# Performance work log

Hardware: AMD Instinct MI355X
Metric: run time of the kernel (lower is better)

Reference implementation:

```python
import jax, jax.numpy as jnp
import numpy as np

B, S, H, OUT, L = 32, 4096, 128, 128, 3


def _log_g(x):
    return jnp.where(x >= 0, jnp.log(jax.nn.relu(x) + 0.5), -jax.nn.softplus(-x))


def _cell(x, Wz, bz, Wh, bh):
    # x: [B, S, Din] -> h: [B, S, H]
    k = x @ Wz.T + bz                              # [B,S,H]
    log_z = -jax.nn.softplus(-k)
    log_coeffs = -jax.nn.softplus(k)
    # h_0 = zeros -> log_g(0) = log(0.5)
    log_h0 = jnp.full((x.shape[0], 1, k.shape[-1]), np.log(0.5), dtype=k.dtype)
    log_tilde_h = _log_g(x @ Wh.T + bh)
    log_values = jnp.concatenate([log_h0, log_z + log_tilde_h], axis=1)  # [B,S+1,H]
    # FAITHFUL to source: cumsum over the FEATURE axis (dim=-1), pad along seq
    a_star = jnp.pad(jnp.cumsum(log_coeffs, axis=-1), ((0, 0), (1, 0), (0, 0)))
    log_h = a_star + jax.lax.cumlogsumexp(log_values - a_star, axis=1)
    # torch forward applies sigmoid to the cell output, then drops the h_0 row
    return jax.nn.sigmoid(jnp.exp(log_h))[:, 1:, :]


def setup_inputs() -> dict:
    key = jax.random.key(0)
    ks = jax.random.split(key, 2 * L + 2)
    inp = {"x": jax.random.normal(ks[0], (B, S), dtype=jnp.float32)}
    for l in range(L):
        din = 1 if l == 0 else H
        inp[f"Wz{l}"] = jax.random.normal(ks[1 + 2 * l], (H, din), dtype=jnp.float32) * 0.02
        inp[f"bz{l}"] = jnp.zeros((H,), dtype=jnp.float32)
        inp[f"Wh{l}"] = jax.random.normal(ks[2 + 2 * l], (H, din), dtype=jnp.float32) * 0.02
        inp[f"bh{l}"] = jnp.zeros((H,), dtype=jnp.float32)
    inp["Wout"] = jax.random.normal(ks[-1], (OUT, H * S), dtype=jnp.float32) * (1.0 / np.sqrt(H * S))
    inp["bout"] = jnp.zeros((OUT,), dtype=jnp.float32)
    return inp


def reference(x, Wz0, bz0, Wh0, bh0, Wz1, bz1, Wh1, bh1, Wz2, bz2, Wh2, bh2, Wout, bout):
    h = x[:, :, None]  # [B,S,1]
    for (Wz, bz, Wh, bh) in ((Wz0, bz0, Wh0, bh0), (Wz1, bz1, Wh1, bh1), (Wz2, bz2, Wh2, bh2)):
        h = _cell(h, Wz, bz, Wh, bh)
    flat = h.reshape(h.shape[0], -1)  # [B, S*H]
    return flat @ Wout.T + bout       # [B, OUT]
```

## Files before the change

kernel.cpp:

```cpp
#include <hip/hip_runtime.h>
#include <hip/hip_bf16.h>
#include <math.h>

#define B_   32
#define S_   4096
#define H_   128
#define OUT_ 128
#define P_   (B_*S_)
#define NC_  64
#define CH_  (S_/NC_)
#define NKS_ 1024
#define KTOT_ (H_*S_)
#define NEGINF_ (-__builtin_inff())
#define HTP_ 136
#define LOGHALF_ (-0.6931471805599453f)

typedef __bf16 bf16x8 __attribute__((ext_vector_type(8)));
typedef float  f32x4  __attribute__((ext_vector_type(4)));
typedef unsigned short ushort8_t __attribute__((ext_vector_type(8)));

__device__ __forceinline__ float sp_(float x) {
  return __logf(1.f + __expf(x));
}
__device__ __forceinline__ float logg_(float x) {
  float t = (x >= 0.f) ? (x + 0.5f) : __builtin_amdgcn_rcpf(1.f + __expf(-x));
  return __logf(t);
}
__device__ __forceinline__ float lae_(float a, float b) {
  float m = fmaxf(a, b);
  float d = -fabsf(a - b);
  return m + __logf(1.f + __expf(d));
}
__device__ __forceinline__ float sigm_(float e) {
  return __builtin_amdgcn_rcpf(1.f + __expf(-e));
}
__device__ __forceinline__ unsigned short f2bf_(float f) {
  unsigned int u = __float_as_uint(f);
  u += 0x7fffu + ((u >> 16) & 1u);
  return (unsigned short)(u >> 16);
}

#define DPPADD_(v, ctrl, rmask) \
  ((v) + __int_as_float(__builtin_amdgcn_update_dpp( \
      0, __float_as_int(v), (ctrl), (rmask), 0xf, true)))
__device__ __forceinline__ float wscan_(float v) {
  v = DPPADD_(v, 0x111, 0xf);
  v = DPPADD_(v, 0x112, 0xf);
  v = DPPADD_(v, 0x114, 0xf);
  v = DPPADD_(v, 0x118, 0xf);
  v = DPPADD_(v, 0x142, 0xa);
  v = DPPADD_(v, 0x143, 0xc);
  return v;
}

__global__ __launch_bounds__(256) void prep0c_kernel(
    const float* __restrict__ x,
    const float* __restrict__ Wz, const float* __restrict__ bz,
    const float* __restrict__ Wh, const float* __restrict__ bh,
    float* __restrict__ Lb, float* __restrict__ A, float* __restrict__ tot,
    const float* __restrict__ Wz1, const float* __restrict__ Wh1,
    const float* __restrict__ Wz2, const float* __restrict__ Wh2,
    unsigned short* __restrict__ Wc1, unsigned short* __restrict__ Wc2)
{
  __shared__ float segw[4][128];
  if (blockIdx.x >= 2048) {
    int idx = (blockIdx.x - 2048) * 256 + threadIdx.x;
    Wc1[idx] = f2bf_(idx < 16384 ? Wz1[idx] : Wh1[idx - 16384]);
    Wc2[idx] = f2bf_(idx < 16384 ? Wz2[idx] : Wh2[idx - 16384]);
    return;
  }
  int lane = threadIdx.x & 63, w = threadIdx.x >> 6;
  float wz0 = Wz[lane], wz1 = Wz[lane + 64];
  float bz0 = bz[lane], bz1 = bz[lane + 64];
  float wh0 = Wh[lane], wh1 = Wh[lane + 64];
  float bh0 = bh[lane], bh1 = bh[lane + 64];
  int blk = blockIdx.x;
  size_t base = (size_t)blk * (CH_ * H_);
  int pos0 = blk * CH_ + w * 16;
  float xv[16];
  #pragma unroll
  for (int j = 0; j < 16; ++j) xv[j] = x[pos0 + j];
  float L0[16], L1[16];
  float r0 = NEGINF_, r1 = NEGINF_;
  #pragma unroll
  for (int j = 0; j < 16; ++j) {
    float k0 = fmaf(xv[j], wz0, bz0), k1 = fmaf(xv[j], wz1, bz1);
    float g0 = fmaf(xv[j], wh0, bh0), g1 = fmaf(xv[j], wh1, bh1);
    float lc0 = -sp_(k0), lc1 = -sp_(k1);
    float lv0 = k0 + lc0 + logg_(g0);
    float lv1 = k1 + lc1 + logg_(g1);
    float s0 = wscan_(lc0);
    float c0 = __shfl(s0, 63, 64);
    float s1 = wscan_(lc1) + c0;
    float u0 = lv0 - s0, u1 = lv1 - s1;
    r0 = lae_(r0, u0); r1 = lae_(r1, u1);
    L0[j] = r0; L1[j] = r1;
    size_t o = base + (size_t)(w * 16 + j) * H_;
    A[o + lane] = s0; A[o + 64 + lane] = s1;
  }
  segw[w][lane] = r0; segw[w][lane + 64] = r1;
  __syncthreads();
  float p0 = NEGINF_, p1 = NEGINF_;
  for (int jj = 0; jj < w; ++jj) {
    p0 = lae_(p0, segw[jj][lane]);
    p1 = lae_(p1, segw[jj][lane + 64]);
  }
  #pragma unroll
  for (int j = 0; j < 16; ++j) {
    size_t o = base + (size_t)(w * 16 + j) * H_;
    Lb[o + lane]      = lae_(p0, L0[j]);
    Lb[o + 64 + lane] = lae_(p1, L1[j]);
  }
  if (w == 0) {
    float q0 = lae_(lae_(segw[0][lane], segw[1][lane]),
                    lae_(segw[2][lane], segw[3][lane]));
    float q1 = lae_(lae_(segw[0][lane + 64], segw[1][lane + 64]),
                    lae_(segw[2][lane + 64], segw[3][lane + 64]));
    tot[(size_t)blk * H_ + lane] = q0;
    tot[(size_t)blk * H_ + 64 + lane] = q1;
  }
}

__global__ __launch_bounds__(256) void kb_kernel(
    const float* __restrict__ totIn,
    const unsigned short* __restrict__ Wc,
    const float* __restrict__ bz, const float* __restrict__ bh,
    float* __restrict__ Lb, float* __restrict__ A,
    float* __restrict__ totOut)
{
  __shared__ unsigned short hT[64][HTP_];
  __shared__ float kg[16][260];
  __shared__ float segw[4][128];
  int tid = threadIdx.x;
  int lane = tid & 63, w = tid >> 6;
  int l15 = lane & 15, quad = lane >> 4;
  int half = tid >> 7, ch = tid & 127;
  int blk = blockIdx.x;
  int cidx = blk & (NC_ - 1);
  size_t base = (size_t)blk * (CH_ * H_);

  {
    const float* tp = totIn + (size_t)(blk - cidx) * H_ + ch;
    float p0 = NEGINF_, p1 = NEGINF_;
    int i = half;
    for (; i + 2 < cidx; i += 4) {
      float a0 = tp[(size_t)i * H_];
      float a1 = tp[(size_t)(i + 2) * H_];
      p0 = lae_(p0, a0); p1 = lae_(p1, a1);
    }
    for (; i < cidx; i += 2) p0 = lae_(p0, tp[(size_t)i * H_]);
    segw[half * 2][ch] = p0; segw[half * 2 + 1][ch] = p1;
  }
  __syncthreads();

  {
    float r = LOGHALF_;
    r = lae_(r, segw[0][ch]); r = lae_(r, segw[1][ch]);
    r = lae_(r, segw[2][ch]); r = lae_(r, segw[3][ch]);
    const float* Lp = Lb + base + (size_t)half * 32 * H_ + ch;
    const float* Ap = A  + base + (size_t)half * 32 * H_ + ch;
    for (int i0 = 0; i0 < 32; i0 += 16) {
      float Lv[16], Av[16];
      #pragma unroll
      for (int i = 0; i < 16; ++i) { Lv[i] = Lp[(i0 + i) * H_]; Av[i] = Ap[(i0 + i) * H_]; }
      #pragma unroll
      for (int i = 0; i < 16; ++i) {
        hT[half * 32 + i0 + i][ch] = f2bf_(sigm_(__expf(Av[i] + lae_(r, Lv[i]))));
      }
    }
  }
  __syncthreads();

  float bz0v = bz[lane], bz1v = bz[lane + 64];
  float bh0v = bh[lane], bh1v = bh[lane + 64];
  float R0 = NEGINF_, R1 = NEGINF_;

  for (int t = 0; t < 4; ++t) {
    f32x4 z = {0.f, 0.f, 0.f, 0.f};
    f32x4 acc[4] = {z, z, z, z};
    #pragma unroll
    for (int kk = 0; kk < 4; ++kk) {
      bf16x8 a = *reinterpret_cast<const bf16x8*>(&hT[t * 16 + l15][kk * 32 + quad * 8]);
      #pragma unroll
      for (int nt = 0; nt < 4; ++nt) {
        int n = w * 64 + nt * 16 + l15;
        bf16x8 bf = *reinterpret_cast<const bf16x8*>(Wc + n * 128 + kk * 32 + quad * 8);
        acc[nt] = __builtin_amdgcn_mfma_f32_16x16x32_bf16(a, bf, acc[nt], 0, 0, 0);
      }
    }
    __syncthreads();
    #pragma unroll
    for (int nt = 0; nt < 4; ++nt) {
      int col = w * 64 + nt * 16 + l15;
      #pragma unroll
      for (int r2 = 0; r2 < 4; ++r2)
        kg[quad * 4 + r2][col] = acc[nt][r2];
    }
    __syncthreads();
    float ll0[4], ll1[4];
    float lr0 = NEGINF_, lr1 = NEGINF_;
    #pragma unroll
    for (int i = 0; i < 4; ++i) {
      int row = w * 4 + i;
      int sIdx = t * 16 + row;
      float k0 = kg[row][lane]        + bz0v;
      float k1 = kg[row][64 + lane]   + bz1v;
      float g0 = kg[row][128 + lane]  + bh0v;
      float g1 = kg[row][192 + lane]  + bh1v;
      float lc0 = -sp_(k0), lc1 = -sp_(k1);
      float lv0 = k0 + lc0 + logg_(g0);
      float lv1 = k1 + lc1 + logg_(g1);
      float s0 = wscan_(lc0);
      float c0 = __shfl(s0, 63, 64);
      float s1 = wscan_(lc1) + c0;
      float u0 = lv0 - s0, u1 = lv1 - s1;
      lr0 = lae_(lr0, u0); lr1 = lae_(lr1, u1);
      ll0[i] = lr0; ll1[i] = lr1;
      size_t o = base + (size_t)sIdx * H_;
      A[o + lane] = s0;  A[o + 64 + lane] = s1;
    }
    segw[w][lane] = lr0; segw[w][lane + 64] = lr1;
    __syncthreads();
    float p0 = R0, p1 = R1;
    for (int jj = 0; jj < w; ++jj) {
      p0 = lae_(p0, segw[jj][lane]);
      p1 = lae_(p1, segw[jj][lane + 64]);
    }
    #pragma unroll
    for (int i = 0; i < 4; ++i) {
      size_t o = base + (size_t)(t * 16 + w * 4 + i) * H_;
      Lb[o + lane]      = lae_(p0, ll0[i]);
      Lb[o + 64 + lane] = lae_(p1, ll1[i]);
    }
    R0 = lae_(R0, lae_(lae_(segw[0][lane], segw[1][lane]),
                       lae_(segw[2][lane], segw[3][lane])));
    R1 = lae_(R1, lae_(lae_(segw[0][lane + 64], segw[1][lane + 64]),
                       lae_(segw[2][lane + 64], segw[3][lane + 64])));
  }

  if (w == 0) {
    totOut[(size_t)blk * H_ + lane] = R0;
    totOut[(size_t)blk * H_ + 64 + lane] = R1;
  }
}

__global__ __launch_bounds__(256) void scan3v2_kernel(
    const float* __restrict__ Lb, const float* __restrict__ A,
    const float* __restrict__ totIn, unsigned short* __restrict__ hbf)
{
  __shared__ float tpart[4][128];
  int tid = threadIdx.x;
  int half = tid >> 7, ch = tid & 127;
  int blk = blockIdx.x;
  int cidx = blk & (NC_ - 1);
  size_t base = (size_t)blk * (CH_ * H_);

  {
    const float* tp = totIn + (size_t)(blk - cidx) * H_ + ch;
    float p0 = NEGINF_, p1 = NEGINF_;
    int i = half;
    for (; i + 2 < cidx; i += 4) {
      float a0 = tp[(size_t)i * H_];
      float a1 = tp[(size_t)(i + 2) * H_];
      p0 = lae_(p0, a0); p1 = lae_(p1, a1);
    }
    for (; i < cidx; i += 2) p0 = lae_(p0, tp[(size_t)i * H_]);
    tpart[half * 2][ch] = p0; tpart[half * 2 + 1][ch] = p1;
  }
  __syncthreads();

  float r = LOGHALF_;
  r = lae_(r, tpart[0][ch]); r = lae_(r, tpart[1][ch]);
  r = lae_(r, tpart[2][ch]); r = lae_(r, tpart[3][ch]);
  const float* Lp = Lb + base + (size_t)half * 32 * H_ + ch;
  const float* Ap = A  + base + (size_t)half * 32 * H_ + ch;
  unsigned short* hp = hbf + base + (size_t)half * 32 * H_ + ch;
  for (int i0 = 0; i0 < 32; i0 += 16) {
    float Lv[16], Av[16];
    #pragma unroll
    for (int i = 0; i < 16; ++i) { Lv[i] = Lp[(i0 + i) * H_]; Av[i] = Ap[(i0 + i) * H_]; }
    #pragma unroll
    for (int i = 0; i < 16; ++i) {
      hp[(size_t)(i0 + i) * H_] = f2bf_(sigm_(__expf(Av[i] + lae_(r, Lv[i]))));
    }
  }
}

__global__ __launch_bounds__(256) void outmm_kernel(
    const unsigned short* __restrict__ hbf,
    const float* __restrict__ Wout,
    float* __restrict__ part)
{
  const int KSL = KTOT_ / NKS_;
  int tid = threadIdx.x, w = tid >> 6, lane = tid & 63;
  int l15 = lane & 15, quad = lane >> 4;
  int k0base = blockIdx.x * KSL;
  f32x4 acc[2][2] = {{{0,0,0,0},{0,0,0,0}},{{0,0,0,0},{0,0,0,0}}};
  for (int ks = 0; ks < KSL; ks += 32) {
    int k0 = k0base + ks;
    bf16x8 a0 = *reinterpret_cast<const bf16x8*>(
        hbf + (size_t)l15 * KTOT_ + k0 + quad * 8);
    bf16x8 a1 = *reinterpret_cast<const bf16x8*>(
        hbf + (size_t)(16 + l15) * KTOT_ + k0 + quad * 8);
    #pragma unroll
    for (int nt = 0; nt < 2; ++nt) {
      int n = w * 32 + nt * 16 + l15;
      const float* wp = Wout + (size_t)n * KTOT_ + k0 + quad * 8;
      float4 wa = *reinterpret_cast<const float4*>(wp);
      float4 wb = *reinterpret_cast<const float4*>(wp + 4);
      ushort8_t tt;
      tt[0] = f2bf_(wa.x); tt[1] = f2bf_(wa.y); tt[2] = f2bf_(wa.z); tt[3] = f2bf_(wa.w);
      tt[4] = f2bf_(wb.x); tt[5] = f2bf_(wb.y); tt[6] = f2bf_(wb.z); tt[7] = f2bf_(wb.w);
      bf16x8 bf = __builtin_bit_cast(bf16x8, tt);
      acc[0][nt] = __builtin_amdgcn_mfma_f32_16x16x32_bf16(a0, bf, acc[0][nt], 0, 0, 0);
      acc[1][nt] = __builtin_amdgcn_mfma_f32_16x16x32_bf16(a1, bf, acc[1][nt], 0, 0, 0);
    }
  }
  float* pp = part + (size_t)blockIdx.x * (B_ * OUT_);
  #pragma unroll
  for (int mt = 0; mt < 2; ++mt)
    #pragma unroll
    for (int nt = 0; nt < 2; ++nt)
      #pragma unroll
      for (int r = 0; r < 4; ++r) {
        int b = mt * 16 + quad * 4 + r;
        int o = w * 32 + nt * 16 + l15;
        pp[b * OUT_ + o] = acc[mt][nt][r];
      }
}

__global__ __launch_bounds__(256) void outred_kernel(
    const float* __restrict__ part, const float* __restrict__ bout,
    float* __restrict__ out)
{
  int w = threadIdx.x >> 6, lane = threadIdx.x & 63;
  int idx = blockIdx.x * 4 + w;
  float s = 0.f;
  for (int wg = lane; wg < NKS_; wg += 64) s += part[(size_t)wg * (B_ * OUT_) + idx];
  #pragma unroll
  for (int d = 32; d; d >>= 1) s += __shfl_down(s, (unsigned)d, 64);
  if (lane == 0) out[idx] = s + bout[idx & (OUT_ - 1)];
}

extern "C" void kernel_launch(void* const* d_in, const int* in_sizes, int n_in,
                              void* d_out, int out_size, void* d_ws, size_t ws_size,
                              hipStream_t stream)
{
  const float* x    = (const float*)d_in[0];
  const float* Wz[3] = {(const float*)d_in[1], (const float*)d_in[5], (const float*)d_in[9]};
  const float* bz[3] = {(const float*)d_in[2], (const float*)d_in[6], (const float*)d_in[10]};
  const float* Wh[3] = {(const float*)d_in[3], (const float*)d_in[7], (const float*)d_in[11]};
  const float* bh[3] = {(const float*)d_in[4], (const float*)d_in[8], (const float*)d_in[12]};
  const float* Wout = (const float*)d_in[13];
  const float* bout = (const float*)d_in[14];
  float* out = (float*)d_out;

  char* ws = (char*)d_ws;
  float*          Lb    = (float*)(ws + 0);
  float*          A     = (float*)(ws + 67108864);
  unsigned short* hbf   = (unsigned short*)(ws + 134217728);
  unsigned short* Wc1   = (unsigned short*)(ws + 167772160);
  unsigned short* Wc2   = (unsigned short*)(ws + 167837696);
  float*          totA  = (float*)(ws + 167903232);
  float*          totB  = (float*)(ws + 168951808);
  float*          part  = (float*)(ws + 0);

  prep0c_kernel<<<B_ * NC_ + 128, 256, 0, stream>>>(
      x, Wz[0], bz[0], Wh[0], bh[0], Lb, A, totA,
      Wz[1], Wh[1], Wz[2], Wh[2], Wc1, Wc2);

  kb_kernel<<<B_ * NC_, 256, 0, stream>>>(totA, Wc1, bz[1], bh[1], Lb, A, totB);
  kb_kernel<<<B_ * NC_, 256, 0, stream>>>(totB, Wc2, bz[2], bh[2], Lb, A, totA);

  scan3v2_kernel<<<B_ * NC_, 256, 0, stream>>>(Lb, A, totA, hbf);

  outmm_kernel<<<NKS_, 256, 0, stream>>>(hbf, Wout, part);
  outred_kernel<<<(B_ * OUT_) / 4, 256, 0, stream>>>(part, bout, out);
}
```

Measured before the change: 681.5 us.

## Recompute layer-0 scan in layer-1 kernel and fuse final scan into output GEMM

The first kernel now only computes per-chunk totals for layer 0 instead of writing the full Lb/A arrays. The layer-1 kernel recomputes the layer-0 cell from x in registers and applies the carry directly. The final-layer scan application moves into the output matmul, which reads Lb/A plus a precomputed per-chunk carry and builds bf16 activations on the fly, removing the hbf round trip. The cost is recomputing layer 0 and reading fp32 Lb/A (twice the bytes of bf16) inside the matmul, plus one extra small carry kernel.

```diff
diff --git a/kernel.cpp b/kernel.cpp
--- a/kernel.cpp
+++ b/kernel.cpp
@@ -53,11 +53,11 @@
   return v;
 }
 
-__global__ __launch_bounds__(256) void prep0c_kernel(
+__global__ __launch_bounds__(256) void tot0c_kernel(
     const float* __restrict__ x,
     const float* __restrict__ Wz, const float* __restrict__ bz,
     const float* __restrict__ Wh, const float* __restrict__ bh,
-    float* __restrict__ Lb, float* __restrict__ A, float* __restrict__ tot,
+    float* __restrict__ tot,
     const float* __restrict__ Wz1, const float* __restrict__ Wh1,
     const float* __restrict__ Wz2, const float* __restrict__ Wh2,
     unsigned short* __restrict__ Wc1, unsigned short* __restrict__ Wc2)
@@ -75,42 +75,23 @@
   float wh0 = Wh[lane], wh1 = Wh[lane + 64];
   float bh0 = bh[lane], bh1 = bh[lane + 64];
   int blk = blockIdx.x;
-  size_t base = (size_t)blk * (CH_ * H_);
   int pos0 = blk * CH_ + w * 16;
-  float xv[16];
-  #pragma unroll
-  for (int j = 0; j < 16; ++j) xv[j] = x[pos0 + j];
-  float L0[16], L1[16];
   float r0 = NEGINF_, r1 = NEGINF_;
   #pragma unroll
   for (int j = 0; j < 16; ++j) {
-    float k0 = fmaf(xv[j], wz0, bz0), k1 = fmaf(xv[j], wz1, bz1);
-    float g0 = fmaf(xv[j], wh0, bh0), g1 = fmaf(xv[j], wh1, bh1);
+    float xv = x[pos0 + j];
+    float k0 = fmaf(xv, wz0, bz0), k1 = fmaf(xv, wz1, bz1);
+    float g0 = fmaf(xv, wh0, bh0), g1 = fmaf(xv, wh1, bh1);
     float lc0 = -sp_(k0), lc1 = -sp_(k1);
     float lv0 = k0 + lc0 + logg_(g0);
     float lv1 = k1 + lc1 + logg_(g1);
     float s0 = wscan_(lc0);
     float c0 = __shfl(s0, 63, 64);
     float s1 = wscan_(lc1) + c0;
-    float u0 = lv0 - s0, u1 = lv1 - s1;
-    r0 = lae_(r0, u0); r1 = lae_(r1, u1);
-    L0[j] = r0; L1[j] = r1;
-    size_t o = base + (size_t)(w * 16 + j) * H_;
-    A[o + lane] = s0; A[o + 64 + lane] = s1;
+    r0 = lae_(r0, lv0 - s0); r1 = lae_(r1, lv1 - s1);
   }
   segw[w][lane] = r0; segw[w][lane + 64] = r1;
   __syncthreads();
-  float p0 = NEGINF_, p1 = NEGINF_;
-  for (int jj = 0; jj < w; ++jj) {
-    p0 = lae_(p0, segw[jj][lane]);
-    p1 = lae_(p1, segw[jj][lane + 64]);
-  }
-  #pragma unroll
-  for (int j = 0; j < 16; ++j) {
-    size_t o = base + (size_t)(w * 16 + j) * H_;
-    Lb[o + lane]      = lae_(p0, L0[j]);
-    Lb[o + 64 + lane] = lae_(p1, L1[j]);
-  }
   if (w == 0) {
     float q0 = lae_(lae_(segw[0][lane], segw[1][lane]),
                     lae_(segw[2][lane], segw[3][lane]));
@@ -121,8 +102,11 @@
   }
 }
 
-__global__ __launch_bounds__(256) void kb_kernel(
-    const float* __restrict__ totIn,
+__global__ __launch_bounds__(256) void kb1_kernel(
+    const float* __restrict__ x,
+    const float* __restrict__ Wz0, const float* __restrict__ bz0,
+    const float* __restrict__ Wh0, const float* __restrict__ bh0,
+    const float* __restrict__ tot0,
     const unsigned short* __restrict__ Wc,
     const float* __restrict__ bz, const float* __restrict__ bh,
     float* __restrict__ Lb, float* __restrict__ A,
@@ -131,42 +115,68 @@
   __shared__ unsigned short hT[64][HTP_];
   __shared__ float kg[16][260];
   __shared__ float segw[4][128];
+  __shared__ float pre[4][128];
   int tid = threadIdx.x;
   int lane = tid & 63, w = tid >> 6;
   int l15 = lane & 15, quad = lane >> 4;
-  int half = tid >> 7, ch = tid & 127;
+  int halfsel = tid >> 7, chh = tid & 127;
   int blk = blockIdx.x;
   int cidx = blk & (NC_ - 1);
   size_t base = (size_t)blk * (CH_ * H_);
 
   {
-    const float* tp = totIn + (size_t)(blk - cidx) * H_ + ch;
+    const float* tp = tot0 + (size_t)(blk - cidx) * H_ + chh;
     float p0 = NEGINF_, p1 = NEGINF_;
-    int i = half;
+    int i = halfsel;
     for (; i + 2 < cidx; i += 4) {
       float a0 = tp[(size_t)i * H_];
       float a1 = tp[(size_t)(i + 2) * H_];
       p0 = lae_(p0, a0); p1 = lae_(p1, a1);
     }
     for (; i < cidx; i += 2) p0 = lae_(p0, tp[(size_t)i * H_]);
-    segw[half * 2][ch] = p0; segw[half * 2 + 1][ch] = p1;
+    pre[halfsel * 2][chh] = p0; pre[halfsel * 2 + 1][chh] = p1;
   }
   __syncthreads();
 
   {
-    float r = LOGHALF_;
-    r = lae_(r, segw[0][ch]); r = lae_(r, segw[1][ch]);
-    r = lae_(r, segw[2][ch]); r = lae_(r, segw[3][ch]);
-    const float* Lp = Lb + base + (size_t)half * 32 * H_ + ch;
-    const float* Ap = A  + base + (size_t)half * 32 * H_ + ch;
-    for (int i0 = 0; i0 < 32; i0 += 16) {
-      float Lv[16], Av[16];
-      #pragma unroll
-      for (int i = 0; i < 16; ++i) { Lv[i] = Lp[(i0 + i) * H_]; Av[i] = Ap[(i0 + i) * H_]; }
-      #pragma unroll
-      for (int i = 0; i < 16; ++i) {
-        hT[half * 32 + i0 + i][ch] = f2bf_(sigm_(__expf(Av[i] + lae_(r, Lv[i]))));
-      }
+    float rA = LOGHALF_, rB = LOGHALF_;
+    rA = lae_(rA, pre[0][lane]); rA = lae_(rA, pre[1][lane]);
+    rA = lae_(rA, pre[2][lane]); rA = lae_(rA, pre[3][lane]);
+    rB = lae_(rB, pre[0][lane + 64]); rB = lae_(rB, pre[1][lane + 64]);
+    rB = lae_(rB, pre[2][lane + 64]); rB = lae_(rB, pre[3][lane + 64]);
+    float wz0 = Wz0[lane], wz1 = Wz0[lane + 64];
+    float bzz0 = bz0[lane], bzz1 = bz0[lane + 64];
+    float wh0 = Wh0[lane], wh1 = Wh0[lane + 64];
+    float bhh0 = bh0[lane], bhh1 = bh0[lane + 64];
+    int pos0 = blk * CH_ + w * 16;
+    float L0[16], L1[16], av0[16], av1[16];
+    float r0 = NEGINF_, r1 = NEGINF_;
+    #pragma unroll
+    for (int j = 0; j < 16; ++j) {
+      float xv = x[pos0 + j];
+      float k0 = fmaf(xv, wz0, bzz0), k1 = fmaf(xv, wz1, bzz1);
+      float g0 = fmaf(xv, wh0, bhh0), g1 = fmaf(xv, wh1, bhh1);
+      float lc0 = -sp_(k0), lc1 = -sp_(k1);
+      float lv0 = k0 + lc0 + logg_(g0);
+      float lv1 = k1 + lc1 + logg_(g1);
+      float s0 = wscan_(lc0);
+      float c0 = __shfl(s0, 63, 64);
+      float s1 = wscan_(lc1) + c0;
+      float u0 = lv0 - s0, u1 = lv1 - s1;
+      r0 = lae_(r0, u0); r1 = lae_(r1, u1);
+      L0[j] = r0; L1[j] = r1; av0[j] = s0; av1[j] = s1;
+    }
+    segw[w][lane] = r0; segw[w][lane + 64] = r1;
+    __syncthreads();
+    float p0 = rA, p1 = rB;
+    for (int jj = 0; jj < w; ++jj) {
+      p0 = lae_(p0, segw[jj][lane]);
+      p1 = lae_(p1, segw[jj][lane + 64]);
+    }
+    #pragma unroll
+    for (int j = 0; j < 16; ++j) {
+      hT[w * 16 + j][lane]      = f2bf_(sigm_(__expf(av0[j] + lae_(p0, L0[j]))));
+      hT[w * 16 + j][lane + 64] = f2bf_(sigm_(__expf(av1[j] + lae_(p1, L1[j]))));
     }
   }
   __syncthreads();
@@ -202,7 +212,6 @@
     #pragma unroll
     for (int i = 0; i < 4; ++i) {
       int row = w * 4 + i;
-      int sIdx = t * 16 + row;
       float k0 = kg[row][lane]        + bz0v;
       float k1 = kg[row][64 + lane]   + bz1v;
       float g0 = kg[row][128 + lane]  + bh0v;
@@ -216,7 +225,7 @@
       float u0 = lv0 - s0, u1 = lv1 - s1;
       lr0 = lae_(lr0, u0); lr1 = lae_(lr1, u1);
       ll0[i] = lr0; ll1[i] = lr1;
-      size_t o = base + (size_t)sIdx * H_;
+      size_t o = base + (size_t)(t * 16 + row) * H_;
       A[o + lane] = s0;  A[o + 64 + lane] = s1;
     }
     segw[w][lane] = lr0; segw[w][lane + 64] = lr1;
@@ -244,12 +253,19 @@
   }
 }
 
-__global__ __launch_bounds__(256) void scan3v2_kernel(
-    const float* __restrict__ Lb, const float* __restrict__ A,
-    const float* __restrict__ totIn, unsigned short* __restrict__ hbf)
-{
-  __shared__ float tpart[4][128];
+__global__ __launch_bounds__(256) void kb2_kernel(
+    const float* __restrict__ totIn,
+    const unsigned short* __restrict__ Wc,
+    const float* __restrict__ bz, const float* __restrict__ bh,
+    float* __restrict__ Lb, float* __restrict__ A,
+    float* __restrict__ totOut)
+{
+  __shared__ unsigned short hT[64][HTP_];
+  __shared__ float kg[16][260];
+  __shared__ float segw[4][128];
   int tid = threadIdx.x;
+  int lane = tid & 63, w = tid >> 6;
+  int l15 = lane & 15, quad = lane >> 4;
   int half = tid >> 7, ch = tid & 127;
   int blk = blockIdx.x;
   int cidx = blk & (NC_ - 1);
@@ -265,43 +281,170 @@
       p0 = lae_(p0, a0); p1 = lae_(p1, a1);
     }
     for (; i < cidx; i += 2) p0 = lae_(p0, tp[(size_t)i * H_]);
-    tpart[half * 2][ch] = p0; tpart[half * 2 + 1][ch] = p1;
+    segw[half * 2][ch] = p0; segw[half * 2 + 1][ch] = p1;
   }
   __syncthreads();
 
-  float r = LOGHALF_;
-  r = lae_(r, tpart[0][ch]); r = lae_(r, tpart[1][ch]);
-  r = lae_(r, tpart[2][ch]); r = lae_(r, tpart[3][ch]);
-  const float* Lp = Lb + base + (size_t)half * 32 * H_ + ch;
-  const float* Ap = A  + base + (size_t)half * 32 * H_ + ch;
-  unsigned short* hp = hbf + base + (size_t)half * 32 * H_ + ch;
-  for (int i0 = 0; i0 < 32; i0 += 16) {
-    float Lv[16], Av[16];
-    #pragma unroll
-    for (int i = 0; i < 16; ++i) { Lv[i] = Lp[(i0 + i) * H_]; Av[i] = Ap[(i0 + i) * H_]; }
-    #pragma unroll
-    for (int i = 0; i < 16; ++i) {
-      hp[(size_t)(i0 + i) * H_] = f2bf_(sigm_(__expf(Av[i] + lae_(r, Lv[i]))));
-    }
-  }
-}
-
-__global__ __launch_bounds__(256) void outmm_kernel(
-    const unsigned short* __restrict__ hbf,
-    const float* __restrict__ Wout,
+  {
+    float r = LOGHALF_;
+    r = lae_(r, segw[0][ch]); r = lae_(r, segw[1][ch]);
+    r = lae_(r, segw[2][ch]); r = lae_(r, segw[3][ch]);
+    const float* Lp = Lb + base + (size_t)half * 32 * H_ + ch;
+    const float* Ap = A  + base + (size_t)half * 32 * H_ + ch;
+    for (int i0 = 0; i0 < 32; i0 += 16) {
+      float Lv[16], Av[16];
+      #pragma unroll
+      for (int i = 0; i < 16; ++i) { Lv[i] = Lp[(i0 + i) * H_]; Av[i] = Ap[(i0 + i) * H_]; }
+      #pragma unroll
+      for (int i = 0; i < 16; ++i) {
+        hT[half * 32 + i0 + i][ch] = f2bf_(sigm_(__expf(Av[i] + lae_(r, Lv[i]))));
+      }
+    }
+  }
+  __syncthreads();
+
+  float bz0v = bz[lane], bz1v = bz[lane + 64];
+  float bh0v = bh[lane], bh1v = bh[lane + 64];
+  float R0 = NEGINF_, R1 = NEGINF_;
+
+  for (int t = 0; t < 4; ++t) {
+    f32x4 z = {0.f, 0.f, 0.f, 0.f};
+    f32x4 acc[4] = {z, z, z, z};
+    #pragma unroll
+    for (int kk = 0; kk < 4; ++kk) {
+      bf16x8 a = *reinterpret_cast<const bf16x8*>(&hT[t * 16 + l15][kk * 32 + quad * 8]);
+      #pragma unroll
+      for (int nt = 0; nt < 4; ++nt) {
+        int n = w * 64 + nt * 16 + l15;
+        bf16x8 bf = *reinterpret_cast<const bf16x8*>(Wc + n * 128 + kk * 32 + quad * 8);
+        acc[nt] = __builtin_amdgcn_mfma_f32_16x16x32_bf16(a, bf, acc[nt], 0, 0, 0);
+      }
+    }
+    __syncthreads();
+    #pragma unroll
+    for (int nt = 0; nt < 4; ++nt) {
+      int col = w * 64 + nt * 16 + l15;
+      #pragma unroll
+      for (int r2 = 0; r2 < 4; ++r2)
+        kg[quad * 4 + r2][col] = acc[nt][r2];
+    }
+    __syncthreads();
+    float ll0[4], ll1[4];
+    float lr0 = NEGINF_, lr1 = NEGINF_;
+    #pragma unroll
+    for (int i = 0; i < 4; ++i) {
+      int row = w * 4 + i;
+      float k0 = kg[row][lane]        + bz0v;
+      float k1 = kg[row][64 + lane]   + bz1v;
+      float g0 = kg[row][128 + lane]  + bh0v;
+      float g1 = kg[row][192 + lane]  + bh1v;
+      float lc0 = -sp_(k0), lc1 = -sp_(k1);
+      float lv0 = k0 + lc0 + logg_(g0);
+      float lv1 = k1 + lc1 + logg_(g1);
+      float s0 = wscan_(lc0);
+      float c0 = __shfl(s0, 63, 64);
+      float s1 = wscan_(lc1) + c0;
+      float u0 = lv0 - s0, u1 = lv1 - s1;
+      lr0 = lae_(lr0, u0); lr1 = lae_(lr1, u1);
+      ll0[i] = lr0; ll1[i] = lr1;
+      size_t o = base + (size_t)(t * 16 + row) * H_;
+      A[o + lane] = s0;  A[o + 64 + lane] = s1;
+    }
+    segw[w][lane] = lr0; segw[w][lane + 64] = lr1;
+    __syncthreads();
+    float p0 = R0, p1 = R1;
+    for (int jj = 0; jj < w; ++jj) {
+      p0 = lae_(p0, segw[jj][lane]);
+      p1 = lae_(p1, segw[jj][lane + 64]);
+    }
+    #pragma unroll
+    for (int i = 0; i < 4; ++i) {
+      size_t o = base + (size_t)(t * 16 + w * 4 + i) * H_;
+      Lb[o + lane]      = lae_(p0, ll0[i]);
+      Lb[o + 64 + lane] = lae_(p1, ll1[i]);
+    }
+    R0 = lae_(R0, lae_(lae_(segw[0][lane], segw[1][lane]),
+                       lae_(segw[2][lane], segw[3][lane])));
+    R1 = lae_(R1, lae_(lae_(segw[0][lane + 64], segw[1][lane + 64]),
+                       lae_(segw[2][lane + 64], segw[3][lane + 64])));
+  }
+
+  if (w == 0) {
+    totOut[(size_t)blk * H_ + lane] = R0;
+    totOut[(size_t)blk * H_ + 64 + lane] = R1;
+  }
+}
+
+__global__ __launch_bounds__(128) void carry2_kernel(
+    const float* __restrict__ tot, float* __restrict__ carry2)
+{
+  int ch = threadIdx.x;
+  int blk = blockIdx.x;
+  int cidx = blk & (NC_ - 1);
+  const float* tp = tot + (size_t)(blk - cidx) * H_ + ch;
+  float p0 = NEGINF_, p1 = NEGINF_;
+  int i = 0;
+  for (; i + 1 < cidx; i += 2) {
+    p0 = lae_(p0, tp[(size_t)i * H_]);
+    p1 = lae_(p1, tp[(size_t)(i + 1) * H_]);
+  }
+  if (i < cidx) p0 = lae_(p0, tp[(size_t)i * H_]);
+  carry2[(size_t)blk * H_ + ch] = lae_(lae_(LOGHALF_, p0), p1);
+}
+
+__global__ __launch_bounds__(256) void outmm2_kernel(
+    const float* __restrict__ Lb, const float* __restrict__ Av,
+    const float* __restrict__ carry2, const float* __restrict__ Wout,
     float* __restrict__ part)
 {
   const int KSL = KTOT_ / NKS_;
   int tid = threadIdx.x, w = tid >> 6, lane = tid & 63;
   int l15 = lane & 15, quad = lane >> 4;
   int k0base = blockIdx.x * KSL;
+  int cchunk = k0base >> 13;
+  const float* cr0 = carry2 + (size_t)(l15 * NC_ + cchunk) * H_;
+  const float* cr1 = carry2 + (size_t)((16 + l15) * NC_ + cchunk) * H_;
   f32x4 acc[2][2] = {{{0,0,0,0},{0,0,0,0}},{{0,0,0,0},{0,0,0,0}}};
   for (int ks = 0; ks < KSL; ks += 32) {
     int k0 = k0base + ks;
-    bf16x8 a0 = *reinterpret_cast<const bf16x8*>(
-        hbf + (size_t)l15 * KTOT_ + k0 + quad * 8);
-    bf16x8 a1 = *reinterpret_cast<const bf16x8*>(
-        hbf + (size_t)(16 + l15) * KTOT_ + k0 + quad * 8);
+    int kq = k0 + quad * 8;
+    int chb = kq & 127;
+    const float* Lp = Lb + (size_t)l15 * KTOT_ + kq;
+    const float* Ap = Av + (size_t)l15 * KTOT_ + kq;
+    float4 lA = *reinterpret_cast<const float4*>(Lp);
+    float4 lB = *reinterpret_cast<const float4*>(Lp + 4);
+    float4 aA = *reinterpret_cast<const float4*>(Ap);
+    float4 aB = *reinterpret_cast<const float4*>(Ap + 4);
+    float4 rA = *reinterpret_cast<const float4*>(cr0 + chb);
+    float4 rB = *reinterpret_cast<const float4*>(cr0 + chb + 4);
+    ushort8_t t0;
+    t0[0] = f2bf_(sigm_(__expf(aA.x + lae_(rA.x, lA.x))));
+    t0[1] = f2bf_(sigm_(__expf(aA.y + lae_(rA.y, lA.y))));
+    t0[2] = f2bf_(sigm_(__expf(aA.z + lae_(rA.z, lA.z))));
+    t0[3] = f2bf_(sigm_(__expf(aA.w + lae_(rA.w, lA.w))));
+    t0[4] = f2bf_(sigm_(__expf(aB.x + lae_(rB.x, lB.x))));
+    t0[5] = f2bf_(sigm_(__expf(aB.y + lae_(rB.y, lB.y))));
+    t0[6] = f2bf_(sigm_(__expf(aB.z + lae_(rB.z, lB.z))));
+    t0[7] = f2bf_(sigm_(__expf(aB.w + lae_(rB.w, lB.w))));
+    bf16x8 a0 = __builtin_bit_cast(bf16x8, t0);
+    const float* Lp1 = Lb + (size_t)(16 + l15) * KTOT_ + kq;
+    const float* Ap1 = Av + (size_t)(16 + l15) * KTOT_ + kq;
+    float4 l1A = *reinterpret_cast<const float4*>(Lp1);
+    float4 l1B = *reinterpret_cast<const float4*>(Lp1 + 4);
+    float4 a1A = *reinterpret_cast<const float4*>(Ap1);
+    float4 a1B = *reinterpret_cast<const float4*>(Ap1 + 4);
+    float4 r1A = *reinterpret_cast<const float4*>(cr1 + chb);
+    float4 r1B = *reinterpret_cast<const float4*>(cr1 + chb + 4);
+    ushort8_t t1;
+    t1[0] = f2bf_(sigm_(__expf(a1A.x + lae_(r1A.x, l1A.x))));
+    t1[1] = f2bf_(sigm_(__expf(a1A.y + lae_(r1A.y, l1A.y))));
+    t1[2] = f2bf_(sigm_(__expf(a1A.z + lae_(r1A.z, l1A.z))));
+    t1[3] = f2bf_(sigm_(__expf(a1A.w + lae_(r1A.w, l1A.w))));
+    t1[4] = f2bf_(sigm_(__expf(a1B.x + lae_(r1B.x, l1B.x))));
+    t1[5] = f2bf_(sigm_(__expf(a1B.y + lae_(r1B.y, l1B.y))));
+    t1[6] = f2bf_(sigm_(__expf(a1B.z + lae_(r1B.z, l1B.z))));
+    t1[7] = f2bf_(sigm_(__expf(a1B.w + lae_(r1B.w, l1B.w))));
+    bf16x8 a1 = __builtin_bit_cast(bf16x8, t1);
     #pragma unroll
     for (int nt = 0; nt < 2; ++nt) {
       int n = w * 32 + nt * 16 + l15;
@@ -358,22 +501,23 @@
   char* ws = (char*)d_ws;
   float*          Lb    = (float*)(ws + 0);
   float*          A     = (float*)(ws + 67108864);
-  unsigned short* hbf   = (unsigned short*)(ws + 134217728);
-  unsigned short* Wc1   = (unsigned short*)(ws + 167772160);
-  unsigned short* Wc2   = (unsigned short*)(ws + 167837696);
-  float*          totA  = (float*)(ws + 167903232);
-  float*          totB  = (float*)(ws + 168951808);
-  float*          part  = (float*)(ws + 0);
-
-  prep0c_kernel<<<B_ * NC_ + 128, 256, 0, stream>>>(
-      x, Wz[0], bz[0], Wh[0], bh[0], Lb, A, totA,
+  float*          part  = (float*)(ws + 134217728);
+  unsigned short* Wc1   = (unsigned short*)(ws + 150994944);
+  unsigned short* Wc2   = (unsigned short*)(ws + 151060480);
+  float*          tot0  = (float*)(ws + 151126016);
+  float*          tot1  = (float*)(ws + 152174592);
+  float*          tot2  = (float*)(ws + 153223168);
+  float*          car2  = (float*)(ws + 154271744);
+
+  tot0c_kernel<<<B_ * NC_ + 128, 256, 0, stream>>>(
+      x, Wz[0], bz[0], Wh[0], bh[0], tot0,
       Wz[1], Wh[1], Wz[2], Wh[2], Wc1, Wc2);
 
-  kb_kernel<<<B_ * NC_, 256, 0, stream>>>(totA, Wc1, bz[1], bh[1], Lb, A, totB);
-  kb_kernel<<<B_ * NC_, 256, 0, stream>>>(totB, Wc2, bz[2], bh[2], Lb, A, totA);
-
-  scan3v2_kernel<<<B_ * NC_, 256, 0, stream>>>(Lb, A, totA, hbf);
-
-  outmm_kernel<<<NKS_, 256, 0, stream>>>(hbf, Wout, part);
+  kb1_kernel<<<B_ * NC_, 256, 0, stream>>>(
+      x, Wz[0], bz[0], Wh[0], bh[0], tot0, Wc1, bz[1], bh[1], Lb, A, tot1);
+  kb2_kernel<<<B_ * NC_, 256, 0, stream>>>(tot1, Wc2, bz[2], bh[2], Lb, A, tot2);
+
+  carry2_kernel<<<B_ * NC_, 128, 0, stream>>>(tot2, car2);
+  outmm2_kernel<<<NKS_, 256, 0, stream>>>(Lb, A, car2, Wout, part);
   outred_kernel<<<(B_ * OUT_) / 4, 256, 0, stream>>>(part, bout, out);
 }
```

New measurement: 798.1 us. +17.1%, slower.
